# Optimization experiments

Hardware: AMD Instinct MI355X
Metric: run time of the kernel (lower is better)

## Reference

```python
import jax, jax.numpy as jnp
import numpy as np

GROUPS = 32
HEADS = 8
EPS = 1e-5


def setup_inputs() -> dict:
    key = jax.random.key(0)
    k1, k2 = jax.random.split(key)
    B, C, H, W = 8, 512, 32, 32
    x = jax.random.normal(k1, (B, C, H, W), dtype=jnp.float32)
    gn_weight = jnp.ones((C,), dtype=jnp.float32)
    gn_bias = jnp.zeros((C,), dtype=jnp.float32)
    w1 = jax.random.normal(k2, (3 * C, C, 1), dtype=jnp.float32) * (C ** -0.5)
    b1 = jnp.zeros((3 * C,), dtype=jnp.float32)
    return {"x": x, "gn_weight": gn_weight, "gn_bias": gn_bias, "w1": w1, "b1": b1}


def reference(x, gn_weight, gn_bias, w1, b1):
    B, C, H, W = x.shape
    T = H * W
    ch = C // HEADS
    # GroupNorm over (C/G, H, W) per group
    xg = x.reshape(B, GROUPS, -1)
    mu = jnp.mean(xg, axis=-1, keepdims=True)
    var = jnp.var(xg, axis=-1, keepdims=True)
    xn = ((xg - mu) * jax.lax.rsqrt(var + EPS)).reshape(B, C, T)
    xn = xn * gn_weight[:, None] + gn_bias[:, None]
    # 1x1 Conv1d -> QKV: [B, 3C, T]
    qkv = jnp.einsum('oc,bct->bot', w1[:, :, 0], xn) + b1[:, None]
    q, k, v = jnp.split(qkv, 3, axis=1)
    q = q.reshape(B, HEADS, ch, T)
    k = k.reshape(B, HEADS, ch, T)
    v = v.reshape(B, HEADS, ch, T)
    scale = ch ** -0.25  # applied to both q and k, per guided-diffusion QKVAttention
    w = jnp.einsum('bhct,bhcs->bhts', q * scale, k * scale)  # [B,H,T,T]
    w = jax.nn.softmax(w, axis=-1)
    a = jnp.einsum('bhts,bhcs->bhct', w, v).reshape(B, C, H, W)
    return a + x
```

## Files before the change

kernel.cpp:

```cpp
#include <hip/hip_runtime.h>
#include <hip/hip_bf16.h>

#define NB 8
#define NC 512
#define NT 1024
#define NHEADS 8
#define NCH 64
#define NGROUPS 32
#define NGC 16

typedef __attribute__((ext_vector_type(4))) unsigned short u16x4;
typedef __attribute__((ext_vector_type(8))) unsigned short u16x8;
typedef __attribute__((ext_vector_type(4))) float f32x4;
typedef __attribute__((ext_vector_type(16))) float f32x16;
typedef __attribute__((ext_vector_type(8))) __bf16 bfv8;

static __device__ __forceinline__ unsigned short f2bf(float f) {
    __bf16 h = (__bf16)f;
    return __builtin_bit_cast(unsigned short, h);
}

static __device__ __forceinline__ unsigned cvtpk(float lo, float hi) {
    unsigned r;
    asm("v_cvt_pk_bf16_f32 %0, %1, %2" : "=v"(r) : "v"(lo), "v"(hi));
    return r;
}

static __device__ __forceinline__ f32x4 mfma_bf16(u16x8 a, u16x8 b, f32x4 c) {
    return __builtin_amdgcn_mfma_f32_16x16x32_bf16(
        __builtin_bit_cast(bfv8, a), __builtin_bit_cast(bfv8, b), c, 0, 0, 0);
}

static __device__ __forceinline__ f32x16 mfma32(u16x8 a, u16x8 b, f32x16 c) {
    return __builtin_amdgcn_mfma_f32_32x32x16_bf16(
        __builtin_bit_cast(bfv8, a), __builtin_bit_cast(bfv8, b), c, 0, 0, 0);
}

static __device__ __forceinline__ void gl_lds16(const unsigned short* g, unsigned short* l) {
    __builtin_amdgcn_global_load_lds(
        (const __attribute__((address_space(1))) unsigned int*)g,
        (__attribute__((address_space(3))) unsigned int*)l, 16, 0, 0);
}

__global__ __launch_bounds__(512) void k_gn_w1(const float* __restrict__ x,
                                               const float* __restrict__ gw,
                                               const float* __restrict__ gb,
                                               const float* __restrict__ w1,
                                               unsigned short* __restrict__ xnT,
                                               unsigned short* __restrict__ w1b) {
    int tid = threadIdx.x;
    if (blockIdx.x >= 256) {
        int i = ((blockIdx.x - 256) * 512 + tid) * 8;
        f32x4 a = *(const f32x4*)(w1 + i);
        f32x4 b = *(const f32x4*)(w1 + i + 4);
        u16x8 o;
#pragma unroll
        for (int j = 0; j < 4; ++j) { o[j] = f2bf(a[j]); o[4 + j] = f2bf(b[j]); }
        *(u16x8*)(w1b + i) = o;
        return;
    }
    int b = blockIdx.x >> 5, g = blockIdx.x & 31;
    int half = tid >> 8, tl = tid & 255;
    int t4 = tl * 4;
    const float* xb = x + ((size_t)(b * NC + g * NGC + half * 8)) * NT;

    f32x4 vv[8];
    float s = 0.f, ss = 0.f;
#pragma unroll
    for (int cc = 0; cc < 8; ++cc) {
        f32x4 v = *(const f32x4*)(xb + cc * NT + t4);
        vv[cc] = v;
#pragma unroll
        for (int i = 0; i < 4; ++i) { s += v[i]; ss += v[i] * v[i]; }
    }
#pragma unroll
    for (int off = 1; off < 64; off <<= 1) { s += __shfl_xor(s, off); ss += __shfl_xor(ss, off); }
    __shared__ float rs_[8], rss[8];
    int w = tid >> 6;
    if ((tid & 63) == 0) { rs_[w] = s; rss[w] = ss; }
    __syncthreads();
    s = 0.f; ss = 0.f;
#pragma unroll
    for (int i = 0; i < 8; ++i) { s += rs_[i]; ss += rss[i]; }
    float mu  = s * (1.f / 16384.f);
    float var = ss * (1.f / 16384.f) - mu * mu;
    float rstd = rsqrtf(var + 1e-5f);

    float wgt[8], bia[8];
#pragma unroll
    for (int cc = 0; cc < 8; ++cc) {
        float ww = gw[g * NGC + half * 8 + cc] * rstd;
        wgt[cc] = ww;
        bia[cc] = gb[g * NGC + half * 8 + cc] - mu * ww;
    }
#pragma unroll
    for (int i = 0; i < 4; ++i) {
        unsigned short o[8];
#pragma unroll
        for (int cc = 0; cc < 8; ++cc) o[cc] = f2bf(vv[cc][i] * wgt[cc] + bia[cc]);
        unsigned short* dst = xnT + ((size_t)(b * NT + t4 + i)) * NC + g * NGC + half * 8;
        *(u16x8*)dst = *(u16x8*)o;
    }
}

__global__ __launch_bounds__(256) void k_qkv_gemm(const unsigned short* __restrict__ w1b,
                                                  const unsigned short* __restrict__ xnT,
                                                  const float* __restrict__ b1,
                                                  unsigned short* __restrict__ q_t,
                                                  unsigned short* __restrict__ k_t,
                                                  unsigned short* __restrict__ vbuf) {
    __shared__ unsigned short As[2 * 128 * 64];
    __shared__ unsigned short Bs[2 * 128 * 64];
    int bid = blockIdx.x;
    int lbid = (bid & 7) * 96 + (bid >> 3);
    int bb = lbid / 96;
    int rr_ = lbid % 96;
    int tm = rr_ >> 3, tn = rr_ & 7;
    int tid = threadIdx.x;
    int l = tid & 63, w = tid >> 6;
    int wm = w >> 1, wn = w & 1;
    int ll = l & 15, lg = l >> 4;
    int rl = l >> 3, sl = l & 7;
    int ssl = sl ^ rl;

    const unsigned short* Ag = w1b + (size_t)(tm * 128) * NC;
    const unsigned short* Bg = xnT + (size_t)(bb * NT + tn * 128) * NC;

    auto STAGE = [&](int k0, int buf) {
        unsigned short* dA = As + buf * 8192 + w * 32 * 64;
        unsigned short* dB = Bs + buf * 8192 + w * 32 * 64;
#pragma unroll
        for (int i = 0; i < 4; ++i) {
            int row = w * 32 + i * 8 + rl;
            gl_lds16(Ag + (size_t)row * NC + k0 + ssl * 8, dA + i * 512);
            gl_lds16(Bg + (size_t)row * NC + k0 + ssl * 8, dB + i * 512);
        }
    };

    f32x4 acc[4][4] = {};
    STAGE(0, 0);
    __syncthreads();
    int cur = 0;
    for (int ks = 0; ks < 8; ++ks) {
        if (ks < 7) STAGE((ks + 1) * 64, cur ^ 1);
        const char* Ac = (const char*)(As + cur * 8192);
        const char* Bc = (const char*)(Bs + cur * 8192);
#pragma unroll
        for (int kk = 0; kk < 2; ++kk) {
            u16x8 af[4], bf[4];
#pragma unroll
            for (int m = 0; m < 4; ++m) {
                int row = wm * 64 + m * 16 + ll;
                af[m] = *(const u16x8*)(Ac + row * 128 + ((kk * 64 + lg * 16) ^ ((row & 7) << 4)));
            }
#pragma unroll
            for (int n = 0; n < 4; ++n) {
                int row = wn * 64 + n * 16 + ll;
                bf[n] = *(const u16x8*)(Bc + row * 128 + ((kk * 64 + lg * 16) ^ ((row & 7) << 4)));
            }
#pragma unroll
            for (int m = 0; m < 4; ++m)
#pragma unroll
                for (int n = 0; n < 4; ++n)
                    acc[m][n] = mfma_bf16(af[m], bf[n], acc[m][n]);
        }
        __syncthreads();
        cur ^= 1;
    }

    if (tm < 8) {
        int qk = tm >> 2;
        int h = (tm & 3) * 2 + wm;
        float sc = qk ? 1.f : 0.125f * 1.44269504088896f;
        int obase = tm * 128 + wm * 64;
        unsigned short* dst = (qk ? k_t : q_t) + ((size_t)(bb * 8 + h)) * NT * NCH;
#pragma unroll
        for (int m = 0; m < 4; ++m) {
#pragma unroll
            for (int n = 0; n < 4; ++n) {
                int t = tn * 128 + wn * 64 + n * 16 + ll;
                u16x4 pk;
#pragma unroll
                for (int r = 0; r < 4; ++r)
                    pk[r] = f2bf((acc[m][n][r] + b1[obase + m * 16 + lg * 4 + r]) * sc);
                *(u16x4*)(dst + (size_t)t * NCH + m * 16 + lg * 4) = pk;
            }
        }
    } else {
        int vcb = (tm - 8) * 128 + wm * 64;
#pragma unroll
        for (int m = 0; m < 4; ++m)
#pragma unroll
            for (int r = 0; r < 4; ++r) {
                int vc = vcb + m * 16 + lg * 4 + r;
                float bias = b1[1024 + vc];
#pragma unroll
                for (int n = 0; n < 4; ++n) {
                    int t = tn * 128 + wn * 64 + n * 16 + ll;
                    vbuf[(size_t)(bb * NC + vc) * NT + t] = f2bf(acc[m][n][r] + bias);
                }
            }
    }
}

__global__ __launch_bounds__(256, 3) void k_attn(const unsigned short* __restrict__ q_t,
                                                 const unsigned short* __restrict__ k_t,
                                                 const unsigned short* __restrict__ vbuf,
                                                 const float* __restrict__ x,
                                                 float* __restrict__ out) {
    __shared__ unsigned char smem[49152];
    unsigned short* sK = (unsigned short*)smem;
    unsigned short* sV = (unsigned short*)(smem + 24576);

    int lbid = ((blockIdx.x & 7) << 6) | (blockIdx.x >> 3);
    int b  = lbid >> 6;
    int h  = (lbid >> 3) & 7;
    int qt = lbid & 7;
    int t0 = qt * 128;

    int tid = threadIdx.x;
    int l = tid & 63, w = tid >> 6;
    int lh = l & 31, hi = l >> 5;
    int rl = l >> 3, sl = l & 7;
    int ssl = sl ^ rl;

    const unsigned short* Qg = q_t + ((size_t)((b * 8 + h) * NT + t0 + w * 32)) * NCH;
    const unsigned short* Kg = k_t + ((size_t)(b * 8 + h)) * NT * NCH;
    const unsigned short* Vg = vbuf + ((size_t)(b * NC + h * NCH)) * NT;

    u16x8 aq[4];
#pragma unroll
    for (int ks = 0; ks < 4; ++ks)
        aq[ks] = *(const u16x8*)(Qg + lh * NCH + ks * 16 + hi * 8);

    f32x16 acc_o[2] = {};
    float rs = 0.f;

    auto STAGE = [&](int s0, int buf) {
        unsigned short* dK = sK + buf * 4096 + w * 1024;
        unsigned short* dV = sV + buf * 4096 + w * 1024;
#pragma unroll
        for (int i = 0; i < 2; ++i) {
            int row = w * 16 + i * 8 + rl;
            gl_lds16(Kg + (size_t)(s0 + row) * NCH + ssl * 8, dK + i * 512);
            gl_lds16(Vg + (size_t)row * NT + s0 + ssl * 8, dV + i * 512);
        }
    };

    STAGE(0, 0);
    STAGE(64, 1);
    STAGE(128, 2);

    for (int tile = 0; tile < 16; ++tile) {
        if (tile < 14)       asm volatile("s_waitcnt vmcnt(8)" ::: "memory");
        else if (tile == 14) asm volatile("s_waitcnt vmcnt(4)" ::: "memory");
        else                 asm volatile("s_waitcnt vmcnt(0)" ::: "memory");
        __builtin_amdgcn_s_barrier();
        __builtin_amdgcn_sched_barrier(0);

        int cur = tile % 3;
        const char* Kc = (const char*)(sK + cur * 4096);
        const char* Vc = (const char*)(sV + cur * 4096);

#pragma unroll
        for (int jt = 0; jt < 2; ++jt) {
            f32x16 sc = {};
#pragma unroll
            for (int ks = 0; ks < 4; ++ks) {
                int row = jt * 32 + lh;
                u16x8 kf = *(const u16x8*)(Kc + row * 128 + ((ks * 32 + hi * 16) ^ ((row & 7) << 4)));
                sc = mfma32(kf, aq[ks], sc);
            }
            float p[16];
#pragma unroll
            for (int r = 0; r < 16; ++r) {
                p[r] = __builtin_amdgcn_exp2f(sc[r]);
                rs += p[r];
            }
#pragma unroll
            for (int eo = 0; eo < 2; ++eo) {
                unsigned A0 = cvtpk(p[8 * eo + 0], p[8 * eo + 1]);
                unsigned A1 = cvtpk(p[8 * eo + 2], p[8 * eo + 3]);
                unsigned B0 = cvtpk(p[8 * eo + 4], p[8 * eo + 5]);
                unsigned B1 = cvtpk(p[8 * eo + 6], p[8 * eo + 7]);
                asm("v_permlane32_swap_b32 %0, %1" : "+v"(A0), "+v"(B0));
                asm("v_permlane32_swap_b32 %0, %1" : "+v"(A1), "+v"(B1));
                union { unsigned u[4]; u16x8 v; } ap_;
                ap_.u[0] = A0; ap_.u[1] = A1; ap_.u[2] = B0; ap_.u[3] = B1;
                int kt = jt * 2 + eo;
#pragma unroll
                for (int ct = 0; ct < 2; ++ct) {
                    int crow = ct * 32 + lh;
                    u16x8 vf = *(const u16x8*)(Vc + crow * 128 + ((kt * 32 + hi * 16) ^ ((crow & 7) << 4)));
                    acc_o[ct] = mfma32(ap_.v, vf, acc_o[ct]);
                }
            }
        }

        __builtin_amdgcn_sched_barrier(0);
        __builtin_amdgcn_s_barrier();
        if (tile < 13) STAGE((tile + 3) * 64, cur);
    }

    float full = rs + __shfl_xor(rs, 32);
    float rinv[16];
#pragma unroll
    for (int reg = 0; reg < 16; ++reg)
        rinv[reg] = 1.f / __shfl(full, (reg & 3) + 8 * (reg >> 2) + 4 * hi);

    char* sO = (char*)(smem + w * 8192);
#pragma unroll
    for (int ct = 0; ct < 2; ++ct) {
        int c = ct * 32 + lh;
        int swz = (c & 7) << 4;
#pragma unroll
        for (int q = 0; q < 4; ++q) {
            f32x4 o4;
#pragma unroll
            for (int r = 0; r < 4; ++r) o4[r] = acc_o[ct][q * 4 + r] * rinv[q * 4 + r];
            *(f32x4*)(sO + c * 128 + ((q * 32 + hi * 16) ^ swz)) = o4;
        }
    }
#pragma unroll
    for (int i2 = 0; i2 < 8; ++i2) {
        int c = i2 * 8 + rl;
        f32x4 o4 = *(const f32x4*)(sO + c * 128 + ((sl * 16) ^ ((c & 7) << 4)));
        size_t gidx = ((size_t)(b * NC + h * NCH + c)) * NT + t0 + w * 32 + sl * 4;
        f32x4 xv = *(const f32x4*)(x + gidx);
#pragma unroll
        for (int q = 0; q < 4; ++q) o4[q] += xv[q];
        *(f32x4*)(out + gidx) = o4;
    }
}

extern "C" void kernel_launch(void* const* d_in, const int* in_sizes, int n_in,
                              void* d_out, int out_size, void* d_ws, size_t ws_size,
                              hipStream_t stream) {
    (void)in_sizes; (void)n_in; (void)out_size; (void)ws_size;
    const float* x  = (const float*)d_in[0];
    const float* gw = (const float*)d_in[1];
    const float* gb = (const float*)d_in[2];
    const float* w1 = (const float*)d_in[3];
    const float* b1 = (const float*)d_in[4];
    float* out = (float*)d_out;

    char* ws = (char*)d_ws;
    unsigned short* w1b  = (unsigned short*)(ws);
    unsigned short* xnT  = (unsigned short*)(ws + (size_t)(2u << 20));
    unsigned short* q_t  = (unsigned short*)(ws + (size_t)(11u << 20));
    unsigned short* k_t  = (unsigned short*)(ws + (size_t)(20u << 20));
    unsigned short* vbuf = (unsigned short*)(ws + (size_t)(29u << 20));

    k_gn_w1<<<dim3(448), dim3(512), 0, stream>>>(x, gw, gb, w1, xnT, w1b);
    k_qkv_gemm<<<dim3(768), dim3(256), 0, stream>>>(w1b, xnT, b1, q_t, k_t, vbuf);
    k_attn<<<dim3(512), dim3(256), 0, stream>>>(q_t, k_t, vbuf, x, out);
}
```

Before: 63.29 us.

## Triple-buffer QKV GEMM with 32-wide K tiles and explicit vmcnt waits

Replaces the double-buffered 64-wide K staging in the QKV projection GEMM with a three-stage ring of 32-wide K tiles. Loads are issued two stages ahead, and the wait before each tile uses explicit s_waitcnt vmcnt counts plus raw barriers instead of __syncthreads. The goal is to hide global-to-LDS load latency behind MFMA work, which only one GEMM kernel of several in the pipeline benefits from. In exchange there are twice as many loop iterations and barriers per K, a new XOR swizzle layout, and correctness now depends on hand-counted vmcnt values.

```diff
diff --git a/kernel.cpp b/kernel.cpp
--- a/kernel.cpp
+++ b/kernel.cpp
@@ -109,8 +109,8 @@
                                                   unsigned short* __restrict__ q_t,
                                                   unsigned short* __restrict__ k_t,
                                                   unsigned short* __restrict__ vbuf) {
-    __shared__ unsigned short As[2 * 128 * 64];
-    __shared__ unsigned short Bs[2 * 128 * 64];
+    __shared__ unsigned short As[3 * 128 * 32];
+    __shared__ unsigned short Bs[3 * 128 * 32];
     int bid = blockIdx.x;
     int lbid = (bid & 7) * 96 + (bid >> 3);
     int bb = lbid / 96;
@@ -120,52 +120,60 @@
     int l = tid & 63, w = tid >> 6;
     int wm = w >> 1, wn = w & 1;
     int ll = l & 15, lg = l >> 4;
-    int rl = l >> 3, sl = l & 7;
-    int ssl = sl ^ rl;
 
     const unsigned short* Ag = w1b + (size_t)(tm * 128) * NC;
     const unsigned short* Bg = xnT + (size_t)(bb * NT + tn * 128) * NC;
 
+    int srow = l >> 2;
+    int sslot = (l & 3) ^ ((l >> 3) & 3);
+
     auto STAGE = [&](int k0, int buf) {
-        unsigned short* dA = As + buf * 8192 + w * 32 * 64;
-        unsigned short* dB = Bs + buf * 8192 + w * 32 * 64;
-#pragma unroll
-        for (int i = 0; i < 4; ++i) {
-            int row = w * 32 + i * 8 + rl;
-            gl_lds16(Ag + (size_t)row * NC + k0 + ssl * 8, dA + i * 512);
-            gl_lds16(Bg + (size_t)row * NC + k0 + ssl * 8, dB + i * 512);
+        unsigned short* dA = As + buf * 4096 + w * 1024;
+        unsigned short* dB = Bs + buf * 4096 + w * 1024;
+#pragma unroll
+        for (int i = 0; i < 2; ++i) {
+            int row = w * 32 + i * 16 + srow;
+            gl_lds16(Ag + (size_t)row * NC + k0 + sslot * 8, dA + i * 512);
+            gl_lds16(Bg + (size_t)row * NC + k0 + sslot * 8, dB + i * 512);
         }
     };
 
     f32x4 acc[4][4] = {};
     STAGE(0, 0);
-    __syncthreads();
-    int cur = 0;
-    for (int ks = 0; ks < 8; ++ks) {
-        if (ks < 7) STAGE((ks + 1) * 64, cur ^ 1);
-        const char* Ac = (const char*)(As + cur * 8192);
-        const char* Bc = (const char*)(Bs + cur * 8192);
-#pragma unroll
-        for (int kk = 0; kk < 2; ++kk) {
-            u16x8 af[4], bf[4];
-#pragma unroll
-            for (int m = 0; m < 4; ++m) {
-                int row = wm * 64 + m * 16 + ll;
-                af[m] = *(const u16x8*)(Ac + row * 128 + ((kk * 64 + lg * 16) ^ ((row & 7) << 4)));
-            }
-#pragma unroll
-            for (int n = 0; n < 4; ++n) {
-                int row = wn * 64 + n * 16 + ll;
-                bf[n] = *(const u16x8*)(Bc + row * 128 + ((kk * 64 + lg * 16) ^ ((row & 7) << 4)));
-            }
-#pragma unroll
-            for (int m = 0; m < 4; ++m)
-#pragma unroll
-                for (int n = 0; n < 4; ++n)
-                    acc[m][n] = mfma_bf16(af[m], bf[n], acc[m][n]);
-        }
-        __syncthreads();
-        cur ^= 1;
+    STAGE(32, 1);
+    STAGE(64, 2);
+
+    int rsw = (ll >> 1) & 3;
+    for (int ks = 0; ks < 16; ++ks) {
+        if (ks < 14)       asm volatile("s_waitcnt vmcnt(8)" ::: "memory");
+        else if (ks == 14) asm volatile("s_waitcnt vmcnt(4)" ::: "memory");
+        else               asm volatile("s_waitcnt vmcnt(0)" ::: "memory");
+        __builtin_amdgcn_s_barrier();
+        __builtin_amdgcn_sched_barrier(0);
+
+        int cur = ks % 3;
+        const char* Ac = (const char*)(As + cur * 4096);
+        const char* Bc = (const char*)(Bs + cur * 4096);
+        u16x8 af[4], bf[4];
+#pragma unroll
+        for (int m = 0; m < 4; ++m) {
+            int row = wm * 64 + m * 16 + ll;
+            af[m] = *(const u16x8*)(Ac + row * 64 + ((lg ^ rsw) * 16));
+        }
+#pragma unroll
+        for (int n = 0; n < 4; ++n) {
+            int row = wn * 64 + n * 16 + ll;
+            bf[n] = *(const u16x8*)(Bc + row * 64 + ((lg ^ rsw) * 16));
+        }
+#pragma unroll
+        for (int m = 0; m < 4; ++m)
+#pragma unroll
+            for (int n = 0; n < 4; ++n)
+                acc[m][n] = mfma_bf16(af[m], bf[n], acc[m][n]);
+
+        __builtin_amdgcn_sched_barrier(0);
+        __builtin_amdgcn_s_barrier();
+        if (ks < 13) STAGE((ks + 3) * 32, cur);
     }
 
     if (tm < 8) {
```

Measured after the change: 66.03 us. 4.3% more time.
